# Kernel optimization log

Hardware: AMD Instinct MI355X
Metric: run time of the kernel (lower is better)

Reference implementation:

```python
import jax, jax.numpy as jnp
import numpy as np

DIM = 2048
H = 16        # num query heads
HK = 2        # num kv heads
D = DIM // H  # head_dim = 128
G = H // HK   # q heads per kv head = 8
SCALE = 1.0 / np.sqrt(D)


def setup_inputs() -> dict:
    key = jax.random.key(0)
    ks = jax.random.split(key, 9)
    xavier = lambda k, fi, fo: jax.random.uniform(k, (fi, fo), jnp.float32,
                                                  -np.sqrt(6.0 / (fi + fo)), np.sqrt(6.0 / (fi + fo)))
    return {
        "x": jax.random.normal(ks[0], (2, 2048, DIM), jnp.float32),
        "Wq": xavier(ks[1], DIM, H * D),  "bq": jnp.zeros((H * D,), jnp.float32),
        "Wk": xavier(ks[2], DIM, HK * D), "bk": jnp.zeros((HK * D,), jnp.float32),
        "Wv": xavier(ks[3], DIM, HK * D), "bv": jnp.zeros((HK * D,), jnp.float32),
        "Wo": xavier(ks[4], H * D, DIM),  "bo": jnp.zeros((DIM,), jnp.float32),
    }


def reference(x, Wq, bq, Wk, bk, Wv, bv, Wo, bo):
    B, T, C = x.shape
    # projections; q grouped as (kv_head, group) so repeat_interleave becomes a broadcast
    q = (x @ Wq + bq).reshape(B, T, HK, G, D)   # [B,T,Hk,G,D]
    k = (x @ Wk + bk).reshape(B, T, HK, D)      # [B,T,Hk,D]
    v = (x @ Wv + bv).reshape(B, T, HK, D)
    # scores: [B,Hk,G,Tq,Tk] — shared K broadcast across the G query heads per kv head
    scores = jnp.einsum('bqhgd,bshd->bhgqs', q, k) * SCALE
    scores = jnp.clip(scores, -100.0, 100.0)
    attn = jax.nn.softmax(scores, axis=-1)
    out = jnp.einsum('bhgqs,bshd->bqhgd', attn, v).reshape(B, T, H * D)
    return out @ Wo + bo
```

## Files before the change

### kernel.cpp

```cpp
#include <hip/hip_runtime.h>
#include <cstdint>

typedef __bf16 bf16x8 __attribute__((ext_vector_type(8)));
typedef float floatx4 __attribute__((ext_vector_type(4)));
typedef float floatx16 __attribute__((ext_vector_type(16)));
typedef unsigned short u16;
typedef unsigned int u32;

#define SCALE2 0.1275434297677098f
#define CLIP2  144.26950408889634f
#define DEFER  8.0f

__device__ __forceinline__ u16 f2bf(float f) {
  union { float f; u32 i; } v; v.f = f;
  u32 r = v.i + 0x7fffu + ((v.i >> 16) & 1u);
  return (u16)(r >> 16);
}

__device__ __forceinline__ u32 cvtpk(float lo, float hi) {
  u32 r;
  asm("v_cvt_pk_bf16_f32 %0, %1, %2" : "=v"(r) : "v"(lo), "v"(hi));
  return r;
}

__device__ __forceinline__ void gll16(const void* g, void* l) {
  __builtin_amdgcn_global_load_lds(
      (const __attribute__((address_space(1))) u32*)g,
      (__attribute__((address_space(3))) u32*)l, 16, 0, 0);
}

__global__ __launch_bounds__(256) void convert_bf16(
    const float* __restrict__ src, u16* __restrict__ dst, int n4) {
  int i = blockIdx.x * 256 + threadIdx.x;
  if (i >= n4) return;
  float4 v = ((const float4*)src)[i];
  ushort4 o;
  o.x = f2bf(v.x); o.y = f2bf(v.y); o.z = f2bf(v.z); o.w = f2bf(v.w);
  ((ushort4*)dst)[i] = o;
}

__global__ __launch_bounds__(256) void transpose_all(
    const float* __restrict__ Wq, const float* __restrict__ Wk,
    const float* __restrict__ Wv, const float* __restrict__ Wo,
    u16* __restrict__ Wqkv_t, u16* __restrict__ Wot) {
  __shared__ u16 tile[32][33];
  const int k0 = blockIdx.x * 32, ny = blockIdx.y;
  const float* src; int ld, nb, n0; u16* dst;
  if (ny < 80) {
    n0 = ny * 32; dst = Wqkv_t;
    if (n0 < 2048)      { src = Wq; ld = 2048; nb = n0; }
    else if (n0 < 2304) { src = Wk; ld = 256;  nb = n0 - 2048; }
    else                { src = Wv; ld = 256;  nb = n0 - 2304; }
  } else {
    n0 = (ny - 80) * 32; dst = Wot; src = Wo; ld = 2048; nb = n0;
  }
  const int tx = threadIdx.x, ty = threadIdx.y;
#pragma unroll
  for (int i = 0; i < 4; i++) {
    int k = ty + i * 8;
    tile[k][tx] = f2bf(src[(size_t)(k0 + k) * ld + nb + tx]);
  }
  __syncthreads();
#pragma unroll
  for (int i = 0; i < 4; i++) {
    int n = ty + i * 8;
    dst[(size_t)(n0 + n) * 2048 + k0 + tx] = tile[tx][n];
  }
}

template <int EPI>
__global__ __launch_bounds__(256) void gemm_bt(
    const u16* __restrict__ A, const u16* __restrict__ Bt,
    const float* __restrict__ bias0, const float* __restrict__ bias1,
    const float* __restrict__ bias2,
    u16* __restrict__ out0, u16* __restrict__ out1, u16* __restrict__ out2,
    float* __restrict__ outf,
    int M, int N, int K) {
  __shared__ u16 As[2][128][32];
  __shared__ u16 Bs[2][128][32];
  const int tid  = threadIdx.x;
  const int w    = tid >> 6, L = tid & 63, ln = L & 15, quad = L >> 4;
  const int m0   = blockIdx.y * 128, n0 = blockIdx.x * 128;
  const int mw   = (w & 1) * 64, nw = (w >> 1) * 64;
  const int sr = w * 32 + (L >> 2), sc = (L & 3) * 8;
  const u16* ga = &A [(size_t)(m0 + sr) * K + sc];
  const u16* gb = &Bt[(size_t)(n0 + sr) * K + sc];
  floatx4 acc[4][4] = {};
  const int nk = K >> 5;

  gll16(ga, &As[0][w * 32][0]);
  gll16(ga + (size_t)16 * K, &As[0][w * 32 + 16][0]);
  gll16(gb, &Bs[0][w * 32][0]);
  gll16(gb + (size_t)16 * K, &Bs[0][w * 32 + 16][0]);

  for (int i = 0; i < nk; i++) {
    const int cur = i & 1;
    __syncthreads();
    if (i + 1 < nk) {
      const int kt = (i + 1) << 5;
      gll16(ga + kt, &As[cur ^ 1][w * 32][0]);
      gll16(ga + (size_t)16 * K + kt, &As[cur ^ 1][w * 32 + 16][0]);
      gll16(gb + kt, &Bs[cur ^ 1][w * 32][0]);
      gll16(gb + (size_t)16 * K + kt, &Bs[cur ^ 1][w * 32 + 16][0]);
    }
    bf16x8 af[4], bf[4];
#pragma unroll
    for (int mb = 0; mb < 4; mb++) af[mb] = *(const bf16x8*)&As[cur][mw + mb * 16 + ln][quad * 8];
#pragma unroll
    for (int nb = 0; nb < 4; nb++) bf[nb] = *(const bf16x8*)&Bs[cur][nw + nb * 16 + ln][quad * 8];
#pragma unroll
    for (int mb = 0; mb < 4; mb++)
#pragma unroll
      for (int nb = 0; nb < 4; nb++)
        acc[mb][nb] = __builtin_amdgcn_mfma_f32_16x16x32_bf16(af[mb], bf[nb], acc[mb][nb], 0, 0, 0);
  }

#pragma unroll
  for (int mb = 0; mb < 4; mb++) {
#pragma unroll
    for (int nb = 0; nb < 4; nb++) {
#pragma unroll
      for (int r = 0; r < 4; r++) {
        const int m = m0 + mw + mb * 16 + quad * 4 + r;
        const int n = n0 + nw + nb * 16 + ln;
        float v = acc[mb][nb][r];
        if constexpr (EPI == 0) {
          if (n < 2048) {
            v = (v + bias0[n]) * SCALE2;
            out0[(size_t)m * 2048 + n] = f2bf(v);
          } else if (n < 2304) {
            const int j = n - 2048;
            v += bias1[j];
            out1[(size_t)m * 256 + j] = f2bf(v);
          } else {
            const int j = n - 2304;
            v += bias2[j];
            const int b = m >> 11, t = m & 2047;
            out2[((size_t)(b * 256 + j)) * 2048 + t] = f2bf(v);
          }
        } else {
          v += bias0[n];
          outf[(size_t)m * (size_t)N + n] = v;
        }
      }
    }
  }
}

__global__ __launch_bounds__(256, 2) void attn_kernel(
    const u16* __restrict__ Q, const u16* __restrict__ K,
    const u16* __restrict__ Vt, u16* __restrict__ O) {
  __shared__ u16 Ksh[2][8 * 512];
  __shared__ u16 Vsh[2][8 * 512];
  const int tid = threadIdx.x;
  const int w = tid >> 6, L = tid & 63;
  const int ln = L & 31, hf = L >> 5;
  const int qt = blockIdx.x, h = blockIdx.y, b = blockIdx.z;
  const int hk = h >> 3;
  const size_t qrow0 = (size_t)b * 2048 + qt * 128 + w * 32;

  const u16* Kbase = K + (size_t)b * 2048 * 256 + hk * 128;
  const u16* Vbase = Vt + (size_t)(b * 2 + hk) * 128 * 2048;

  const u16* gK[2];
  const u16* gV[2];
#pragma unroll
  for (int j = 0; j < 2; j++) {
    const int fK = 2 * w + j;
    gK[j] = Kbase + (size_t)ln * 256 + fK * 16 + hf * 8;
    const int fV = 2 * w + j, db = fV >> 1, ks = fV & 1;
    gV[j] = Vbase + (size_t)(db * 32 + ln) * 2048 + ks * 16 + hf * 8;
  }

  bf16x8 qf[8];
#pragma unroll
  for (int kc = 0; kc < 8; kc++)
    qf[kc] = *(const bf16x8*)&Q[(qrow0 + ln) * 2048 + h * 128 + kc * 16 + hf * 8];

  floatx16 oT[4] = {};
  float mrow = -1e30f, lrow = 0.f;

  auto issue = [&](int tile, int bufi) {
#pragma unroll
    for (int j = 0; j < 2; j++) {
      gll16(gK[j] + (size_t)tile * 32 * 256, &Ksh[bufi][(2 * w + j) * 512]);
      gll16(gV[j] + (size_t)tile * 32,       &Vsh[bufi][(2 * w + j) * 512]);
    }
  };

  auto qkt = [&](floatx16& sf, const u16* kb) {
#pragma unroll
    for (int r = 0; r < 16; r++) sf[r] = 0.f;
#pragma unroll
    for (int kc = 0; kc < 8; kc++) {
      bf16x8 kf = *(const bf16x8*)&kb[kc * 512 + L * 8];
      sf = __builtin_amdgcn_mfma_f32_32x32x16_bf16(kf, qf[kc], sf, 0, 0, 0);
    }
  };

  auto softmax = [&](floatx16& sf) {
#pragma unroll
    for (int r = 0; r < 16; r++)
      sf[r] = __builtin_amdgcn_fmed3f(sf[r], -CLIP2, CLIP2);
    float t8[8];
#pragma unroll
    for (int r = 0; r < 8; r++) t8[r] = fmaxf(sf[r], sf[r + 8]);
#pragma unroll
    for (int d = 4; d >= 1; d >>= 1)
#pragma unroll
      for (int r = 0; r < d; r++) t8[r] = fmaxf(t8[r], t8[r + d]);
    const float mx = fmaxf(t8[0], __shfl_xor(t8[0], 32));
    const bool need = __ballot(mx > mrow + DEFER) != 0;
    float mn = mrow, alpha = 1.f;
    if (need) {
      mn = fmaxf(mrow, mx);
      alpha = __builtin_amdgcn_exp2f(mrow - mn);
      mrow = mn;
    }
#pragma unroll
    for (int r = 0; r < 16; r++)
      sf[r] = __builtin_amdgcn_exp2f(sf[r] - mn);
    float s8[8];
#pragma unroll
    for (int r = 0; r < 8; r++) s8[r] = sf[r] + sf[r + 8];
#pragma unroll
    for (int d = 4; d >= 1; d >>= 1)
#pragma unroll
      for (int r = 0; r < d; r++) s8[r] += s8[r + d];
    const float s = s8[0] + __shfl_xor(s8[0], 32);
    if (need) {
      lrow = lrow * alpha + s;
#pragma unroll
      for (int db = 0; db < 4; db++)
#pragma unroll
        for (int r = 0; r < 16; r++) oT[db][r] *= alpha;
    } else {
      lrow += s;
    }
  };

  auto pv = [&](floatx16& sf, const u16* vb) {
#pragma unroll
    for (int ks = 0; ks < 2; ks++) {
      const int s8p = ks * 8;
      u32 cA0 = cvtpk(sf[s8p + 0], sf[s8p + 1]);
      u32 cA1 = cvtpk(sf[s8p + 2], sf[s8p + 3]);
      u32 cB0 = cvtpk(sf[s8p + 4], sf[s8p + 5]);
      u32 cB1 = cvtpk(sf[s8p + 6], sf[s8p + 7]);
      asm("v_permlane32_swap_b32 %0, %1" : "+v"(cA0), "+v"(cB0));
      asm("v_permlane32_swap_b32 %0, %1" : "+v"(cA1), "+v"(cB1));
      union { u32 u[4]; bf16x8 v; } pb;
      pb.u[0] = cA0; pb.u[1] = cA1; pb.u[2] = cB0; pb.u[3] = cB1;
#pragma unroll
      for (int db = 0; db < 4; db++) {
        bf16x8 vf = *(const bf16x8*)&vb[(db * 2 + ks) * 512 + L * 8];
        oT[db] = __builtin_amdgcn_mfma_f32_32x32x16_bf16(vf, pb.v, oT[db], 0, 0, 0);
      }
    }
  };

  floatx16 sfA, sfB;

  issue(0, 0);
  __syncthreads();
  issue(1, 1);
  qkt(sfA, &Ksh[0][0]);

  for (int t = 0; t < 64; t += 2) {
    softmax(sfA);
    __syncthreads();
    __builtin_amdgcn_s_setprio(1);
    qkt(sfB, &Ksh[1][0]);
    pv(sfA, &Vsh[0][0]);
    __builtin_amdgcn_s_setprio(0);
    __syncthreads();
    if (t + 2 < 64) issue(t + 2, 0);
    softmax(sfB);
    __syncthreads();
    __builtin_amdgcn_s_setprio(1);
    if (t + 2 < 64) qkt(sfA, &Ksh[0][0]);
    pv(sfB, &Vsh[1][0]);
    __builtin_amdgcn_s_setprio(0);
    __syncthreads();
    if (t + 3 < 64) issue(t + 3, 1);
  }

  const float inv = 1.f / lrow;
  u16* orow = O + (qrow0 + ln) * 2048 + h * 128;
#pragma unroll
  for (int db = 0; db < 4; db++) {
#pragma unroll
    for (int g = 0; g < 4; g++) {
      uint2 st;
      st.x = cvtpk(oT[db][g * 4 + 0] * inv, oT[db][g * 4 + 1] * inv);
      st.y = cvtpk(oT[db][g * 4 + 2] * inv, oT[db][g * 4 + 3] * inv);
      *(uint2*)&orow[db * 32 + g * 8 + hf * 4] = st;
    }
  }
}

extern "C" void kernel_launch(void* const* d_in, const int* in_sizes, int n_in,
                              void* d_out, int out_size, void* d_ws, size_t ws_size,
                              hipStream_t stream) {
  const float* x  = (const float*)d_in[0];
  const float* Wq = (const float*)d_in[1];
  const float* bq = (const float*)d_in[2];
  const float* Wk = (const float*)d_in[3];
  const float* bk = (const float*)d_in[4];
  const float* Wv = (const float*)d_in[5];
  const float* bv = (const float*)d_in[6];
  const float* Wo = (const float*)d_in[7];
  const float* bo = (const float*)d_in[8];
  float* out = (float*)d_out;

  char* ws = (char*)d_ws;
  u16* xb     = (u16*)(ws);
  u16* Ob     = (u16*)(ws);
  u16* Wqkv_t = (u16*)(ws + 16777216);
  u16* Wot    = (u16*)(ws + 27262976);
  u16* Qb     = (u16*)(ws + 35651584);
  u16* Kb     = (u16*)(ws + 52428800);
  u16* Vtb    = (u16*)(ws + 54525952);
  (void)in_sizes; (void)n_in; (void)out_size; (void)ws_size;

  convert_bf16<<<8192, 256, 0, stream>>>(x, xb, 2097152);

  transpose_all<<<dim3(64, 144), dim3(32, 8), 0, stream>>>(
      Wq, Wk, Wv, Wo, Wqkv_t, Wot);

  gemm_bt<0><<<dim3(20, 32), 256, 0, stream>>>(
      xb, Wqkv_t, bq, bk, bv, Qb, Kb, Vtb, nullptr, 4096, 2560, 2048);

  attn_kernel<<<dim3(16, 16, 2), 256, 0, stream>>>(Qb, Kb, Vtb, Ob);

  gemm_bt<1><<<dim3(16, 32), 256, 0, stream>>>(
      Ob, Wot, bo, nullptr, nullptr, nullptr, nullptr, nullptr, out, 4096, 2048, 2048);
}
```

Before: 332.2 us.

## Deepen attention K/V prefetch to four LDS buffers with vmcnt-based barriers

```diff
diff --git a/kernel.cpp b/kernel.cpp
--- a/kernel.cpp
+++ b/kernel.cpp
@@ -28,6 +28,12 @@
       (const __attribute__((address_space(1))) u32*)g,
       (__attribute__((address_space(3))) u32*)l, 16, 0, 0);
 }
+
+#define VMBAR(N)                                                   \
+  do {                                                             \
+    asm volatile("s_waitcnt vmcnt(" #N ")" ::: "memory");          \
+    __builtin_amdgcn_s_barrier();                                  \
+  } while (0)
 
 __global__ __launch_bounds__(256) void convert_bf16(
     const float* __restrict__ src, u16* __restrict__ dst, int n4) {
@@ -150,8 +156,8 @@
 __global__ __launch_bounds__(256, 2) void attn_kernel(
     const u16* __restrict__ Q, const u16* __restrict__ K,
     const u16* __restrict__ Vt, u16* __restrict__ O) {
-  __shared__ u16 Ksh[2][8 * 512];
-  __shared__ u16 Vsh[2][8 * 512];
+  __shared__ u16 Ksh[4][8 * 512];
+  __shared__ u16 Vsh[4][8 * 512];
   const int tid = threadIdx.x;
   const int w = tid >> 6, L = tid & 63;
   const int ln = L & 31, hf = L >> 5;
@@ -188,12 +194,12 @@
     }
   };
 
-  auto qkt = [&](floatx16& sf, const u16* kb) {
+  auto qkt = [&](floatx16& sf, int bufi) {
 #pragma unroll
     for (int r = 0; r < 16; r++) sf[r] = 0.f;
 #pragma unroll
     for (int kc = 0; kc < 8; kc++) {
-      bf16x8 kf = *(const bf16x8*)&kb[kc * 512 + L * 8];
+      bf16x8 kf = *(const bf16x8*)&Ksh[bufi][kc * 512 + L * 8];
       sf = __builtin_amdgcn_mfma_f32_32x32x16_bf16(kf, qf[kc], sf, 0, 0, 0);
     }
   };
@@ -239,7 +245,7 @@
     }
   };
 
-  auto pv = [&](floatx16& sf, const u16* vb) {
+  auto pv = [&](floatx16& sf, int bufi) {
 #pragma unroll
     for (int ks = 0; ks < 2; ks++) {
       const int s8p = ks * 8;
@@ -253,7 +259,7 @@
       pb.u[0] = cA0; pb.u[1] = cA1; pb.u[2] = cB0; pb.u[3] = cB1;
 #pragma unroll
       for (int db = 0; db < 4; db++) {
-        bf16x8 vf = *(const bf16x8*)&vb[(db * 2 + ks) * 512 + L * 8];
+        bf16x8 vf = *(const bf16x8*)&Vsh[bufi][(db * 2 + ks) * 512 + L * 8];
         oT[db] = __builtin_amdgcn_mfma_f32_32x32x16_bf16(vf, pb.v, oT[db], 0, 0, 0);
       }
     }
@@ -261,29 +267,28 @@
 
   floatx16 sfA, sfB;
 
-  issue(0, 0);
-  __syncthreads();
-  issue(1, 1);
-  qkt(sfA, &Ksh[0][0]);
-
-  for (int t = 0; t < 64; t += 2) {
-    softmax(sfA);
-    __syncthreads();
-    __builtin_amdgcn_s_setprio(1);
-    qkt(sfB, &Ksh[1][0]);
-    pv(sfA, &Vsh[0][0]);
-    __builtin_amdgcn_s_setprio(0);
-    __syncthreads();
-    if (t + 2 < 64) issue(t + 2, 0);
-    softmax(sfB);
-    __syncthreads();
-    __builtin_amdgcn_s_setprio(1);
-    if (t + 2 < 64) qkt(sfA, &Ksh[0][0]);
-    pv(sfB, &Vsh[1][0]);
-    __builtin_amdgcn_s_setprio(0);
-    __syncthreads();
-    if (t + 3 < 64) issue(t + 3, 1);
-  }
+  issue(0, 0); issue(1, 1); issue(2, 2);
+  VMBAR(8);
+  qkt(sfA, 0);
+
+  for (int t = 0; t < 60; t += 4) {
+    softmax(sfA); VMBAR(4); issue(t + 3, 3);
+    __builtin_amdgcn_s_setprio(1); qkt(sfB, 1); pv(sfA, 0); __builtin_amdgcn_s_setprio(0);
+    softmax(sfB); VMBAR(4); issue(t + 4, 0);
+    __builtin_amdgcn_s_setprio(1); qkt(sfA, 2); pv(sfB, 1); __builtin_amdgcn_s_setprio(0);
+    softmax(sfA); VMBAR(4); issue(t + 5, 1);
+    __builtin_amdgcn_s_setprio(1); qkt(sfB, 3); pv(sfA, 2); __builtin_amdgcn_s_setprio(0);
+    softmax(sfB); VMBAR(4); issue(t + 6, 2);
+    __builtin_amdgcn_s_setprio(1); qkt(sfA, 0); pv(sfB, 3); __builtin_amdgcn_s_setprio(0);
+  }
+  softmax(sfA); VMBAR(4); issue(63, 3);
+  __builtin_amdgcn_s_setprio(1); qkt(sfB, 1); pv(sfA, 0); __builtin_amdgcn_s_setprio(0);
+  softmax(sfB); VMBAR(4);
+  __builtin_amdgcn_s_setprio(1); qkt(sfA, 2); pv(sfB, 1); __builtin_amdgcn_s_setprio(0);
+  softmax(sfA); VMBAR(0);
+  __builtin_amdgcn_s_setprio(1); qkt(sfB, 3); pv(sfA, 2); __builtin_amdgcn_s_setprio(0);
+  softmax(sfB);
+  pv(sfB, 3);
 
   const float inv = 1.f / lrow;
   u16* orow = O + (qrow0 + ln) * 2048 + h * 128;
```

After: 327.8 us. Within noise of the previous version (-1.3%).
